# Kernel tuning notes

Hardware: AMD Instinct MI355X
Metric: run time of the kernel (lower is better)

The kernel has to match this reference:

```python
import jax, jax.numpy as jnp
import numpy as np

E = 768
H = 12
D = E // H  # head_dim = 64
EPS = 1e-6
SCALE = D ** -0.5


def _l2norm(x, eps=EPS):
    # torch F.normalize: x / clamp_min(||x||_2, eps)
    n = jnp.sqrt(jnp.sum(x * x, axis=-1, keepdims=True))
    return x / jnp.maximum(n, eps)


def setup_inputs() -> dict:
    key = jax.random.key(0)
    ks = jax.random.split(key, 12)
    B, S = 2, 2048
    w = lambda k: jax.random.normal(k, (E, E), dtype=jnp.float32) * 0.02
    b = lambda k: jax.random.normal(k, (E,), dtype=jnp.float32) * 0.02
    return {
        "query": jax.random.normal(ks[0], (B, S, E), dtype=jnp.float32),
        "key": jax.random.normal(ks[1], (B, S, E), dtype=jnp.float32),
        "value": jax.random.normal(ks[2], (B, S, E), dtype=jnp.float32),
        "Wq": w(ks[3]), "bq": b(ks[4]),
        "Wk": w(ks[5]), "bk": b(ks[6]),
        "Wv": w(ks[7]), "bv": b(ks[8]),
        "Wo": w(ks[9]), "bo": b(ks[10]),
    }


def reference(query, key, value, Wq, bq, Wk, bk, Wv, bv, Wo, bo):
    B, T, _ = query.shape
    S = key.shape[1]
    # nn.Linear: x @ W.T + b; then split heads -> [B, H, S, D]
    split = lambda x, L: x.reshape(B, L, H, D).transpose(0, 2, 1, 3)
    q = split(query @ Wq.T + bq, T)
    k = split(key @ Wk.T + bk, S)
    v = split(value @ Wv.T + bv, S)
    q = _l2norm(q)
    k = _l2norm(k)
    scores = jnp.einsum("bhtd,bhsd->bhts", q, k) * SCALE
    attn = jax.nn.softmax(scores, axis=-1)
    ctx = jnp.einsum("bhts,bhsd->bhtd", attn, v)
    ctx = ctx.transpose(0, 2, 1, 3).reshape(B, T, E)
    return ctx @ Wo.T + bo
```

## Files before the change

kernel.cpp:

```cpp
#include <hip/hip_runtime.h>
#include <hip/hip_bf16.h>

#define EE 768
#define HH 12
#define DD 64
#define BB 2
#define SS 2048
#define MM (BB*SS)

typedef short short8 __attribute__((ext_vector_type(8)));
typedef float f32x4 __attribute__((ext_vector_type(4)));

static __device__ __forceinline__ unsigned short f2bf(float f) {
    unsigned int u = __float_as_uint(f);
    u += 0x7fffu + ((u >> 16) & 1u);
    return (unsigned short)(u >> 16);
}

static __device__ __forceinline__ int swz(int row, int chunk) {
    return row * 128 + ((chunk ^ (row & 7)) << 4);
}

__global__ __launch_bounds__(256) void qkv_mfma_kernel(
    const float* __restrict__ xq, const float* __restrict__ xk, const float* __restrict__ xv,
    const float* __restrict__ Wq, const float* __restrict__ bq,
    const float* __restrict__ Wk, const float* __restrict__ bk,
    const float* __restrict__ Wv, const float* __restrict__ bv,
    unsigned short* __restrict__ qo, unsigned short* __restrict__ ko,
    unsigned short* __restrict__ vo)
{
    __shared__ short As[128 * 64];
    __shared__ short Bs[64 * 64];
    __shared__ float ssq[2][128];

    const int tid = threadIdx.x;
    const int bm  = blockIdx.x * 128;
    const int by  = blockIdx.y;
    const int proj = by / 12;
    const int h    = by % 12;
    const int n0r  = h * 64;

    const float* x    = (proj == 0) ? xq : (proj == 1) ? xk : xv;
    const float* W    = (proj == 0) ? Wq : (proj == 1) ? Wk : Wv;
    const float* bias = (proj == 0) ? bq : (proj == 1) ? bk : bv;

    const int w  = tid >> 6;
    const int l  = tid & 63;
    const int c  = l & 15;
    const int g  = l >> 4;
    const int wm = w >> 1;
    const int wn = w & 1;

    f32x4 acc[4][2] = {};

    for (int kt = 0; kt < EE; kt += 64) {
        __syncthreads();
        #pragma unroll
        for (int i = 0; i < 4; ++i) {
            const int cid = tid + 256 * i;
            const int row = cid >> 3, ch = cid & 7;
            const float* ga = x + (size_t)(bm + row) * EE + kt + ch * 8;
            float4 f0 = *(const float4*)ga;
            float4 f1 = *(const float4*)(ga + 4);
            short8 pk;
            pk[0]=f2bf(f0.x); pk[1]=f2bf(f0.y); pk[2]=f2bf(f0.z); pk[3]=f2bf(f0.w);
            pk[4]=f2bf(f1.x); pk[5]=f2bf(f1.y); pk[6]=f2bf(f1.z); pk[7]=f2bf(f1.w);
            *(short8*)((char*)As + swz(row, ch)) = pk;
        }
        #pragma unroll
        for (int i = 0; i < 2; ++i) {
            const int cid = tid + 256 * i;
            const int row = cid >> 3, ch = cid & 7;
            const float* ga = W + (size_t)(n0r + row) * EE + kt + ch * 8;
            float4 f0 = *(const float4*)ga;
            float4 f1 = *(const float4*)(ga + 4);
            short8 pk;
            pk[0]=f2bf(f0.x); pk[1]=f2bf(f0.y); pk[2]=f2bf(f0.z); pk[3]=f2bf(f0.w);
            pk[4]=f2bf(f1.x); pk[5]=f2bf(f1.y); pk[6]=f2bf(f1.z); pk[7]=f2bf(f1.w);
            *(short8*)((char*)Bs + swz(row, ch)) = pk;
        }
        __syncthreads();

        #pragma unroll
        for (int ks = 0; ks < 2; ++ks) {
            short8 bf[2], af[4];
            #pragma unroll
            for (int nt = 0; nt < 2; ++nt) {
                const int row = wn * 32 + nt * 16 + c;
                bf[nt] = *(const short8*)((const char*)Bs + swz(row, ks * 4 + g));
            }
            #pragma unroll
            for (int mt = 0; mt < 4; ++mt) {
                const int row = wm * 64 + mt * 16 + c;
                af[mt] = *(const short8*)((const char*)As + swz(row, ks * 4 + g));
            }
            #pragma unroll
            for (int mt = 0; mt < 4; ++mt)
                #pragma unroll
                for (int nt = 0; nt < 2; ++nt)
                    acc[mt][nt] = __builtin_amdgcn_mfma_f32_16x16x32_bf16(
                        af[mt], bf[nt], acc[mt][nt], 0, 0, 0);
        }
    }
    __syncthreads();

    float bb[2];
    #pragma unroll
    for (int nt = 0; nt < 2; ++nt) bb[nt] = bias[n0r + wn * 32 + nt * 16 + c];

    const int bidx = bm >> 11;
    const int sbase = bm & (SS - 1);

    if (proj < 2) {
        f32x4 vr[4][2];
        f32x4 ssp[4];
        #pragma unroll
        for (int mt = 0; mt < 4; ++mt) {
            #pragma unroll
            for (int nt = 0; nt < 2; ++nt)
                #pragma unroll
                for (int j = 0; j < 4; ++j)
                    vr[mt][nt][j] = acc[mt][nt][j] + bb[nt];
            #pragma unroll
            for (int j = 0; j < 4; ++j)
                ssp[mt][j] = vr[mt][0][j]*vr[mt][0][j] + vr[mt][1][j]*vr[mt][1][j];
            #pragma unroll
            for (int j = 0; j < 4; ++j) {
                float s = ssp[mt][j];
                #pragma unroll
                for (int msk = 1; msk < 16; msk <<= 1) s += __shfl_xor(s, msk);
                ssp[mt][j] = s;
            }
        }
        if (c == 0) {
            #pragma unroll
            for (int mt = 0; mt < 4; ++mt)
                #pragma unroll
                for (int j = 0; j < 4; ++j)
                    ssq[wn][wm * 64 + mt * 16 + g * 4 + j] = ssp[mt][j];
        }
        __syncthreads();
        unsigned short* dst = (proj == 0) ? qo : ko;
        const float fold = (proj == 0) ? 0.125f : 1.0f;
        #pragma unroll
        for (int mt = 0; mt < 4; ++mt) {
            #pragma unroll
            for (int j = 0; j < 4; ++j) {
                const int rloc = wm * 64 + mt * 16 + g * 4 + j;
                const float ss = ssq[0][rloc] + ssq[1][rloc];
                const float inv = fold / fmaxf(sqrtf(ss), 1e-6f);
                const size_t base =
                    ((size_t)(bidx * HH + h) * SS + sbase + rloc) * DD;
                #pragma unroll
                for (int nt = 0; nt < 2; ++nt)
                    dst[base + wn * 32 + nt * 16 + c] = f2bf(vr[mt][nt][j] * inv);
            }
        }
    } else {
        #pragma unroll
        for (int mt = 0; mt < 4; ++mt)
            #pragma unroll
            for (int nt = 0; nt < 2; ++nt)
                #pragma unroll
                for (int j = 0; j < 4; ++j) {
                    const int row = wm * 64 + mt * 16 + g * 4 + j;
                    const int col = wn * 32 + nt * 16 + c;
                    As[row * 64 + col] = (short)f2bf(acc[mt][nt][j] + bb[nt]);
                }
        __syncthreads();
        const int d  = tid & 63;
        const int sb = (tid >> 6) * 32;
        unsigned short* dstp = vo + ((size_t)(bidx * HH + h) * DD + d) * SS + sbase + sb;
        #pragma unroll
        for (int grp = 0; grp < 4; ++grp) {
            unsigned int wds[4];
            #pragma unroll
            for (int e = 0; e < 4; ++e) {
                unsigned short u0 = (unsigned short)As[(sb + grp * 8 + 2 * e)     * 64 + d];
                unsigned short u1 = (unsigned short)As[(sb + grp * 8 + 2 * e + 1) * 64 + d];
                wds[e] = (unsigned int)u0 | ((unsigned int)u1 << 16);
            }
            int4 pk = make_int4((int)wds[0], (int)wds[1], (int)wds[2], (int)wds[3]);
            *(int4*)(dstp + grp * 8) = pk;
        }
    }
}

__global__ __launch_bounds__(256) void attn_mfma_kernel(
    const unsigned short* __restrict__ q, const unsigned short* __restrict__ k,
    const unsigned short* __restrict__ vT, unsigned short* __restrict__ ctx)
{
    __shared__ short Ks[64 * 64];
    __shared__ short Vs[64 * 64];
    __shared__ short Ps[4 * 16 * 64];

    const int tid = threadIdx.x;
    const int bh  = blockIdx.y;
    const int w   = tid >> 6;
    const int l   = tid & 63;
    const int c   = l & 15;
    const int g   = l >> 4;
    const int qr0 = blockIdx.x * 64 + w * 16;

    const unsigned short* qg = q + ((size_t)bh * SS + qr0 + c) * DD;
    short8 aq[2];
    aq[0] = *(const short8*)(qg + g * 8);
    aq[1] = *(const short8*)(qg + 32 + g * 8);

    short* Psw = Ps + w * (16 * 64);

    f32x4 o[4] = {};
    f32x4 lr = {0.f, 0.f, 0.f, 0.f};

    for (int s0 = 0; s0 < SS; s0 += 64) {
        __syncthreads();
        #pragma unroll
        for (int i = 0; i < 2; ++i) {
            const int cid = tid + 256 * i;
            const int key = cid >> 3, ch = cid & 7;
            int4 kv4 = *(const int4*)(k + ((size_t)bh * SS + s0 + key) * DD + ch * 8);
            *(int4*)((char*)Ks + swz(key, ch)) = kv4;
        }
        #pragma unroll
        for (int i = 0; i < 2; ++i) {
            const int cid = tid + 256 * i;
            const int d = cid >> 3, ch = cid & 7;
            int4 vv4 = *(const int4*)(vT + ((size_t)bh * DD + d) * SS + s0 + ch * 8);
            *(int4*)((char*)Vs + swz(d, ch)) = vv4;
        }
        __syncthreads();

        f32x4 sc[4] = {};
        #pragma unroll
        for (int ks = 0; ks < 2; ++ks)
            #pragma unroll
            for (int nt = 0; nt < 4; ++nt) {
                const int row = nt * 16 + c;
                short8 kf = *(const short8*)((const char*)Ks + swz(row, ks * 4 + g));
                sc[nt] = __builtin_amdgcn_mfma_f32_16x16x32_bf16(aq[ks], kf, sc[nt], 0, 0, 0);
            }

        f32x4 p[4];
        #pragma unroll
        for (int nt = 0; nt < 4; ++nt)
            #pragma unroll
            for (int j = 0; j < 4; ++j)
                p[nt][j] = __expf(sc[nt][j]);
        f32x4 rs;
        #pragma unroll
        for (int j = 0; j < 4; ++j) {
            float r = p[0][j] + p[1][j] + p[2][j] + p[3][j];
            #pragma unroll
            for (int msk = 1; msk < 16; msk <<= 1) r += __shfl_xor(r, msk);
            rs[j] = r;
        }
        #pragma unroll
        for (int j = 0; j < 4; ++j) lr[j] += rs[j];

        #pragma unroll
        for (int nt = 0; nt < 4; ++nt)
            #pragma unroll
            for (int j = 0; j < 4; ++j) {
                const int row = g * 4 + j;
                const int elem = row * 64 + (((nt * 2 + (c >> 3)) ^ (row & 7)) << 3) + (c & 7);
                Psw[elem] = (short)f2bf(p[nt][j]);
            }

        #pragma unroll
        for (int ks = 0; ks < 2; ++ks) {
            short8 pa = *(const short8*)((const char*)Psw + swz(c, ks * 4 + g));
            #pragma unroll
            for (int dt = 0; dt < 4; ++dt) {
                const int row = dt * 16 + c;
                short8 vf = *(const short8*)((const char*)Vs + swz(row, ks * 4 + g));
                o[dt] = __builtin_amdgcn_mfma_f32_16x16x32_bf16(pa, vf, o[dt], 0, 0, 0);
            }
        }
    }

    const int bidx = bh / HH, h = bh % HH;
    f32x4 invl;
    #pragma unroll
    for (int j = 0; j < 4; ++j) invl[j] = 1.0f / lr[j];
    #pragma unroll
    for (int j = 0; j < 4; ++j) {
        const int sg = qr0 + g * 4 + j;
        unsigned short* op = ctx + ((size_t)bidx * SS + sg) * EE + h * DD + c;
        #pragma unroll
        for (int dt = 0; dt < 4; ++dt)
            op[dt * 16] = f2bf(o[dt][j] * invl[j]);
    }
}

__global__ __launch_bounds__(256) void out_mfma_kernel(
    const unsigned short* __restrict__ A, const float* __restrict__ W,
    const float* __restrict__ bias, float* __restrict__ out)
{
    __shared__ short As[128 * 64];
    __shared__ short Bs[64 * 64];

    const int tid = threadIdx.x;
    const int bm  = blockIdx.x * 128;
    const int n0  = blockIdx.y * 64;

    const int w  = tid >> 6;
    const int l  = tid & 63;
    const int c  = l & 15;
    const int g  = l >> 4;
    const int wm = w >> 1;
    const int wn = w & 1;

    f32x4 acc[4][2] = {};

    for (int kt = 0; kt < EE; kt += 64) {
        __syncthreads();
        #pragma unroll
        for (int i = 0; i < 4; ++i) {
            const int cid = tid + 256 * i;
            const int row = cid >> 3, ch = cid & 7;
            int4 a8 = *(const int4*)(A + (size_t)(bm + row) * EE + kt + ch * 8);
            *(int4*)((char*)As + swz(row, ch)) = a8;
        }
        #pragma unroll
        for (int i = 0; i < 2; ++i) {
            const int cid = tid + 256 * i;
            const int row = cid >> 3, ch = cid & 7;
            const float* ga = W + (size_t)(n0 + row) * EE + kt + ch * 8;
            float4 f0 = *(const float4*)ga;
            float4 f1 = *(const float4*)(ga + 4);
            short8 pk;
            pk[0]=f2bf(f0.x); pk[1]=f2bf(f0.y); pk[2]=f2bf(f0.z); pk[3]=f2bf(f0.w);
            pk[4]=f2bf(f1.x); pk[5]=f2bf(f1.y); pk[6]=f2bf(f1.z); pk[7]=f2bf(f1.w);
            *(short8*)((char*)Bs + swz(row, ch)) = pk;
        }
        __syncthreads();

        #pragma unroll
        for (int ks = 0; ks < 2; ++ks) {
            short8 bf[2], af[4];
            #pragma unroll
            for (int nt = 0; nt < 2; ++nt) {
                const int row = wn * 32 + nt * 16 + c;
                bf[nt] = *(const short8*)((const char*)Bs + swz(row, ks * 4 + g));
            }
            #pragma unroll
            for (int mt = 0; mt < 4; ++mt) {
                const int row = wm * 64 + mt * 16 + c;
                af[mt] = *(const short8*)((const char*)As + swz(row, ks * 4 + g));
            }
            #pragma unroll
            for (int mt = 0; mt < 4; ++mt)
                #pragma unroll
                for (int nt = 0; nt < 2; ++nt)
                    acc[mt][nt] = __builtin_amdgcn_mfma_f32_16x16x32_bf16(
                        af[mt], bf[nt], acc[mt][nt], 0, 0, 0);
        }
    }

    float bb[2];
    #pragma unroll
    for (int nt = 0; nt < 2; ++nt) bb[nt] = bias[n0 + wn * 32 + nt * 16 + c];

    #pragma unroll
    for (int mt = 0; mt < 4; ++mt)
        #pragma unroll
        for (int j = 0; j < 4; ++j) {
            const int row = bm + wm * 64 + mt * 16 + g * 4 + j;
            float* op = out + (size_t)row * EE + n0 + wn * 32 + c;
            #pragma unroll
            for (int nt = 0; nt < 2; ++nt)
                op[nt * 16] = acc[mt][nt][j] + bb[nt];
        }
}

extern "C" void kernel_launch(void* const* d_in, const int* in_sizes, int n_in,
                              void* d_out, int out_size, void* d_ws, size_t ws_size,
                              hipStream_t stream)
{
    const float* query = (const float*)d_in[0];
    const float* key   = (const float*)d_in[1];
    const float* value = (const float*)d_in[2];
    const float* Wq = (const float*)d_in[3];
    const float* bq = (const float*)d_in[4];
    const float* Wk = (const float*)d_in[5];
    const float* bk = (const float*)d_in[6];
    const float* Wv = (const float*)d_in[7];
    const float* bv = (const float*)d_in[8];
    const float* Wo = (const float*)d_in[9];
    const float* bo = (const float*)d_in[10];
    float* out = (float*)d_out;

    const size_t NQ = (size_t)BB * HH * SS * DD;
    unsigned short* qws  = (unsigned short*)d_ws;
    unsigned short* kws  = qws + NQ;
    unsigned short* vtws = kws + NQ;
    unsigned short* ctx  = vtws + NQ;

    qkv_mfma_kernel<<<dim3(MM/128, 36), 256, 0, stream>>>(
        query, key, value, Wq, bq, Wk, bk, Wv, bv, qws, kws, vtws);
    attn_mfma_kernel<<<dim3(SS/64, BB*HH), 256, 0, stream>>>(qws, kws, vtws, ctx);
    out_mfma_kernel<<<dim3(MM/128, EE/64), 256, 0, stream>>>(ctx, Wo, bo, out);
}
```

Measured before the change: 246.2 us.

## Pre-convert inputs to bf16, use direct global-to-LDS loads, widen attention waves

Adds separate kernels that convert activations and all four weight matrices to bf16 up front, so the GEMM kernels stop redoing fp32-to-bf16 conversion for every tile they reload. The GEMM and attention tile loads now use global_load_lds with an XOR-swizzled source column, replacing the register round-trip. The attention kernel drops to 128 threads, with each wave handling 32 query rows so each K/V fragment feeds two MFMAs. The cost is two extra launches, extra workspace traffic for the bf16 copies, and fewer waves per attention block.

```diff
diff --git a/kernel.cpp b/kernel.cpp
--- a/kernel.cpp
+++ b/kernel.cpp
@@ -7,6 +7,8 @@
 #define BB 2
 #define SS 2048
 #define MM (BB*SS)
+#define NT (MM*EE)
+#define NW (EE*EE)
 
 typedef short short8 __attribute__((ext_vector_type(8)));
 typedef float f32x4 __attribute__((ext_vector_type(4)));
@@ -17,15 +19,51 @@
     return (unsigned short)(u >> 16);
 }
 
+static __device__ __forceinline__ void gl16(const void* g, void* l) {
+    __builtin_amdgcn_global_load_lds(
+        (const __attribute__((address_space(1))) unsigned int*)g,
+        (__attribute__((address_space(3))) unsigned int*)l, 16, 0, 0);
+}
+
 static __device__ __forceinline__ int swz(int row, int chunk) {
     return row * 128 + ((chunk ^ (row & 7)) << 4);
 }
 
+__global__ __launch_bounds__(256) void cvt_x_kernel(
+    const float* __restrict__ a0, const float* __restrict__ a1, const float* __restrict__ a2,
+    unsigned short* __restrict__ o0, unsigned short* __restrict__ o1, unsigned short* __restrict__ o2)
+{
+    const float* s = (blockIdx.y == 0) ? a0 : (blockIdx.y == 1) ? a1 : a2;
+    unsigned short* d = (blockIdx.y == 0) ? o0 : (blockIdx.y == 1) ? o1 : o2;
+    const int idx = blockIdx.x * 256 + threadIdx.x;
+    float4 f = ((const float4*)s)[idx];
+    ushort4 u;
+    u.x = f2bf(f.x); u.y = f2bf(f.y); u.z = f2bf(f.z); u.w = f2bf(f.w);
+    ((ushort4*)d)[idx] = u;
+}
+
+__global__ __launch_bounds__(256) void cvt_w_kernel(
+    const float* __restrict__ a0, const float* __restrict__ a1,
+    const float* __restrict__ a2, const float* __restrict__ a3,
+    unsigned short* __restrict__ o0, unsigned short* __restrict__ o1,
+    unsigned short* __restrict__ o2, unsigned short* __restrict__ o3)
+{
+    const int y = blockIdx.y;
+    const float* s = (y == 0) ? a0 : (y == 1) ? a1 : (y == 2) ? a2 : a3;
+    unsigned short* d = (y == 0) ? o0 : (y == 1) ? o1 : (y == 2) ? o2 : o3;
+    const int idx = blockIdx.x * 256 + threadIdx.x;
+    float4 f = ((const float4*)s)[idx];
+    ushort4 u;
+    u.x = f2bf(f.x); u.y = f2bf(f.y); u.z = f2bf(f.z); u.w = f2bf(f.w);
+    ((ushort4*)d)[idx] = u;
+}
+
 __global__ __launch_bounds__(256) void qkv_mfma_kernel(
-    const float* __restrict__ xq, const float* __restrict__ xk, const float* __restrict__ xv,
-    const float* __restrict__ Wq, const float* __restrict__ bq,
-    const float* __restrict__ Wk, const float* __restrict__ bk,
-    const float* __restrict__ Wv, const float* __restrict__ bv,
+    const unsigned short* __restrict__ xq, const unsigned short* __restrict__ xk,
+    const unsigned short* __restrict__ xv,
+    const unsigned short* __restrict__ Wq, const float* __restrict__ bq,
+    const unsigned short* __restrict__ Wk, const float* __restrict__ bk,
+    const unsigned short* __restrict__ Wv, const float* __restrict__ bv,
     unsigned short* __restrict__ qo, unsigned short* __restrict__ ko,
     unsigned short* __restrict__ vo)
 {
@@ -40,9 +78,9 @@
     const int h    = by % 12;
     const int n0r  = h * 64;
 
-    const float* x    = (proj == 0) ? xq : (proj == 1) ? xk : xv;
-    const float* W    = (proj == 0) ? Wq : (proj == 1) ? Wk : Wv;
-    const float* bias = (proj == 0) ? bq : (proj == 1) ? bk : bv;
+    const unsigned short* x = (proj == 0) ? xq : (proj == 1) ? xk : xv;
+    const unsigned short* W = (proj == 0) ? Wq : (proj == 1) ? Wk : Wv;
+    const float* bias       = (proj == 0) ? bq : (proj == 1) ? bk : bv;
 
     const int w  = tid >> 6;
     const int l  = tid & 63;
@@ -50,6 +88,8 @@
     const int g  = l >> 4;
     const int wm = w >> 1;
     const int wn = w & 1;
+    const int lr8 = l >> 3;
+    const int lc8 = (l & 7) ^ lr8;
 
     f32x4 acc[4][2] = {};
 
@@ -57,49 +97,35 @@
         __syncthreads();
         #pragma unroll
         for (int i = 0; i < 4; ++i) {
-            const int cid = tid + 256 * i;
-            const int row = cid >> 3, ch = cid & 7;
-            const float* ga = x + (size_t)(bm + row) * EE + kt + ch * 8;
-            float4 f0 = *(const float4*)ga;
-            float4 f1 = *(const float4*)(ga + 4);
-            short8 pk;
-            pk[0]=f2bf(f0.x); pk[1]=f2bf(f0.y); pk[2]=f2bf(f0.z); pk[3]=f2bf(f0.w);
-            pk[4]=f2bf(f1.x); pk[5]=f2bf(f1.y); pk[6]=f2bf(f1.z); pk[7]=f2bf(f1.w);
-            *(short8*)((char*)As + swz(row, ch)) = pk;
+            const int t = w * 4 + i;
+            const int row = t * 8 + lr8;
+            gl16(x + (size_t)(bm + row) * EE + kt + lc8 * 8,
+                 (unsigned short*)As + t * 512);
         }
         #pragma unroll
         for (int i = 0; i < 2; ++i) {
-            const int cid = tid + 256 * i;
-            const int row = cid >> 3, ch = cid & 7;
-            const float* ga = W + (size_t)(n0r + row) * EE + kt + ch * 8;
-            float4 f0 = *(const float4*)ga;
-            float4 f1 = *(const float4*)(ga + 4);
-            short8 pk;
-            pk[0]=f2bf(f0.x); pk[1]=f2bf(f0.y); pk[2]=f2bf(f0.z); pk[3]=f2bf(f0.w);
-            pk[4]=f2bf(f1.x); pk[5]=f2bf(f1.y); pk[6]=f2bf(f1.z); pk[7]=f2bf(f1.w);
-            *(short8*)((char*)Bs + swz(row, ch)) = pk;
+            const int t = w * 2 + i;
+            const int row = t * 8 + lr8;
+            gl16(W + (size_t)(n0r + row) * EE + kt + lc8 * 8,
+                 (unsigned short*)Bs + t * 512);
         }
         __syncthreads();
 
         #pragma unroll
         for (int ks = 0; ks < 2; ++ks) {
-            short8 bf[2], af[4];
-            #pragma unroll
-            for (int nt = 0; nt < 2; ++nt) {
-                const int row = wn * 32 + nt * 16 + c;
-                bf[nt] = *(const short8*)((const char*)Bs + swz(row, ks * 4 + g));
-            }
-            #pragma unroll
-            for (int mt = 0; mt < 4; ++mt) {
-                const int row = wm * 64 + mt * 16 + c;
-                af[mt] = *(const short8*)((const char*)As + swz(row, ks * 4 + g));
-            }
+            short8 bfr[2], afr[4];
+            #pragma unroll
+            for (int nt = 0; nt < 2; ++nt)
+                bfr[nt] = *(const short8*)((const char*)Bs + swz(wn * 32 + nt * 16 + c, ks * 4 + g));
+            #pragma unroll
+            for (int mt = 0; mt < 4; ++mt)
+                afr[mt] = *(const short8*)((const char*)As + swz(wm * 64 + mt * 16 + c, ks * 4 + g));
             #pragma unroll
             for (int mt = 0; mt < 4; ++mt)
                 #pragma unroll
                 for (int nt = 0; nt < 2; ++nt)
                     acc[mt][nt] = __builtin_amdgcn_mfma_f32_16x16x32_bf16(
-                        af[mt], bf[nt], acc[mt][nt], 0, 0, 0);
+                        afr[mt], bfr[nt], acc[mt][nt], 0, 0, 0);
         }
     }
     __syncthreads();
@@ -108,7 +134,7 @@
     #pragma unroll
     for (int nt = 0; nt < 2; ++nt) bb[nt] = bias[n0r + wn * 32 + nt * 16 + c];
 
-    const int bidx = bm >> 11;
+    const int bidx  = bm >> 11;
     const int sbase = bm & (SS - 1);
 
     if (proj < 2) {
@@ -186,13 +212,13 @@
     }
 }
 
-__global__ __launch_bounds__(256) void attn_mfma_kernel(
+__global__ __launch_bounds__(128) void attn_mfma_kernel(
     const unsigned short* __restrict__ q, const unsigned short* __restrict__ k,
     const unsigned short* __restrict__ vT, unsigned short* __restrict__ ctx)
 {
     __shared__ short Ks[64 * 64];
     __shared__ short Vs[64 * 64];
-    __shared__ short Ps[4 * 16 * 64];
+    __shared__ short Ps[2 * 32 * 64];
 
     const int tid = threadIdx.x;
     const int bh  = blockIdx.y;
@@ -200,100 +226,108 @@
     const int l   = tid & 63;
     const int c   = l & 15;
     const int g   = l >> 4;
-    const int qr0 = blockIdx.x * 64 + w * 16;
-
-    const unsigned short* qg = q + ((size_t)bh * SS + qr0 + c) * DD;
-    short8 aq[2];
-    aq[0] = *(const short8*)(qg + g * 8);
-    aq[1] = *(const short8*)(qg + 32 + g * 8);
-
-    short* Psw = Ps + w * (16 * 64);
-
-    f32x4 o[4] = {};
-    f32x4 lr = {0.f, 0.f, 0.f, 0.f};
+    const int lr8 = l >> 3;
+    const int lc8 = (l & 7) ^ lr8;
+    const int qr0 = blockIdx.x * 64 + w * 32;
+
+    short8 aq[2][2];
+    #pragma unroll
+    for (int m = 0; m < 2; ++m) {
+        const unsigned short* qg = q + ((size_t)bh * SS + qr0 + m * 16 + c) * DD;
+        aq[m][0] = *(const short8*)(qg + g * 8);
+        aq[m][1] = *(const short8*)(qg + 32 + g * 8);
+    }
+
+    short* Psw = Ps + w * (32 * 64);
+    f32x4 o[2][4] = {};
+    f32x4 lsum[2] = {};
 
     for (int s0 = 0; s0 < SS; s0 += 64) {
         __syncthreads();
         #pragma unroll
-        for (int i = 0; i < 2; ++i) {
-            const int cid = tid + 256 * i;
-            const int key = cid >> 3, ch = cid & 7;
-            int4 kv4 = *(const int4*)(k + ((size_t)bh * SS + s0 + key) * DD + ch * 8);
-            *(int4*)((char*)Ks + swz(key, ch)) = kv4;
-        }
-        #pragma unroll
-        for (int i = 0; i < 2; ++i) {
-            const int cid = tid + 256 * i;
-            const int d = cid >> 3, ch = cid & 7;
-            int4 vv4 = *(const int4*)(vT + ((size_t)bh * DD + d) * SS + s0 + ch * 8);
-            *(int4*)((char*)Vs + swz(d, ch)) = vv4;
-        }
-        __syncthreads();
-
-        f32x4 sc[4] = {};
+        for (int i = 0; i < 4; ++i) {
+            const int t = w * 4 + i;
+            gl16(k + ((size_t)bh * SS + s0 + t * 8 + lr8) * DD + lc8 * 8,
+                 (unsigned short*)Ks + t * 512);
+        }
+        #pragma unroll
+        for (int i = 0; i < 4; ++i) {
+            const int t = w * 4 + i;
+            gl16(vT + ((size_t)bh * DD + t * 8 + lr8) * SS + s0 + lc8 * 8,
+                 (unsigned short*)Vs + t * 512);
+        }
+        __syncthreads();
+
+        f32x4 sc[2][4] = {};
         #pragma unroll
         for (int ks = 0; ks < 2; ++ks)
             #pragma unroll
             for (int nt = 0; nt < 4; ++nt) {
-                const int row = nt * 16 + c;
-                short8 kf = *(const short8*)((const char*)Ks + swz(row, ks * 4 + g));
-                sc[nt] = __builtin_amdgcn_mfma_f32_16x16x32_bf16(aq[ks], kf, sc[nt], 0, 0, 0);
-            }
-
-        f32x4 p[4];
-        #pragma unroll
-        for (int nt = 0; nt < 4; ++nt)
-            #pragma unroll
-            for (int j = 0; j < 4; ++j)
-                p[nt][j] = __expf(sc[nt][j]);
-        f32x4 rs;
+                short8 kf = *(const short8*)((const char*)Ks + swz(nt * 16 + c, ks * 4 + g));
+                #pragma unroll
+                for (int m = 0; m < 2; ++m)
+                    sc[m][nt] = __builtin_amdgcn_mfma_f32_16x16x32_bf16(
+                        aq[m][ks], kf, sc[m][nt], 0, 0, 0);
+            }
+
+        #pragma unroll
+        for (int m = 0; m < 2; ++m) {
+            f32x4 p[4];
+            #pragma unroll
+            for (int nt = 0; nt < 4; ++nt)
+                #pragma unroll
+                for (int j = 0; j < 4; ++j)
+                    p[nt][j] = __expf(sc[m][nt][j]);
+            #pragma unroll
+            for (int j = 0; j < 4; ++j) {
+                float r = p[0][j] + p[1][j] + p[2][j] + p[3][j];
+                #pragma unroll
+                for (int msk = 1; msk < 16; msk <<= 1) r += __shfl_xor(r, msk);
+                lsum[m][j] += r;
+            }
+            #pragma unroll
+            for (int nt = 0; nt < 4; ++nt)
+                #pragma unroll
+                for (int j = 0; j < 4; ++j) {
+                    const int row = m * 16 + g * 4 + j;
+                    const int ch  = (nt * 2 + (c >> 3)) ^ (row & 7);
+                    Psw[row * 64 + (ch << 3) + (c & 7)] = (short)f2bf(p[nt][j]);
+                }
+        }
+
+        #pragma unroll
+        for (int ks = 0; ks < 2; ++ks) {
+            short8 pa[2];
+            #pragma unroll
+            for (int m = 0; m < 2; ++m)
+                pa[m] = *(const short8*)((const char*)Psw + swz(m * 16 + c, ks * 4 + g));
+            #pragma unroll
+            for (int dt = 0; dt < 4; ++dt) {
+                short8 vf = *(const short8*)((const char*)Vs + swz(dt * 16 + c, ks * 4 + g));
+                #pragma unroll
+                for (int m = 0; m < 2; ++m)
+                    o[m][dt] = __builtin_amdgcn_mfma_f32_16x16x32_bf16(
+                        pa[m], vf, o[m][dt], 0, 0, 0);
+            }
+        }
+    }
+
+    const int bidx = bh / HH, h = bh % HH;
+    #pragma unroll
+    for (int m = 0; m < 2; ++m)
         #pragma unroll
         for (int j = 0; j < 4; ++j) {
-            float r = p[0][j] + p[1][j] + p[2][j] + p[3][j];
-            #pragma unroll
-            for (int msk = 1; msk < 16; msk <<= 1) r += __shfl_xor(r, msk);
-            rs[j] = r;
-        }
-        #pragma unroll
-        for (int j = 0; j < 4; ++j) lr[j] += rs[j];
-
-        #pragma unroll
-        for (int nt = 0; nt < 4; ++nt)
-            #pragma unroll
-            for (int j = 0; j < 4; ++j) {
-                const int row = g * 4 + j;
-                const int elem = row * 64 + (((nt * 2 + (c >> 3)) ^ (row & 7)) << 3) + (c & 7);
-                Psw[elem] = (short)f2bf(p[nt][j]);
-            }
-
-        #pragma unroll
-        for (int ks = 0; ks < 2; ++ks) {
-            short8 pa = *(const short8*)((const char*)Psw + swz(c, ks * 4 + g));
-            #pragma unroll
-            for (int dt = 0; dt < 4; ++dt) {
-                const int row = dt * 16 + c;
-                short8 vf = *(const short8*)((const char*)Vs + swz(row, ks * 4 + g));
-                o[dt] = __builtin_amdgcn_mfma_f32_16x16x32_bf16(pa, vf, o[dt], 0, 0, 0);
-            }
-        }
-    }
-
-    const int bidx = bh / HH, h = bh % HH;
-    f32x4 invl;
-    #pragma unroll
-    for (int j = 0; j < 4; ++j) invl[j] = 1.0f / lr[j];
-    #pragma unroll
-    for (int j = 0; j < 4; ++j) {
-        const int sg = qr0 + g * 4 + j;
-        unsigned short* op = ctx + ((size_t)bidx * SS + sg) * EE + h * DD + c;
-        #pragma unroll
-        for (int dt = 0; dt < 4; ++dt)
-            op[dt * 16] = f2bf(o[dt][j] * invl[j]);
-    }
+            const float inv = 1.0f / lsum[m][j];
+            const int sg = qr0 + m * 16 + g * 4 + j;
+            unsigned short* op = ctx + ((size_t)bidx * SS + sg) * EE + h * DD + c;
+            #pragma unroll
+            for (int dt = 0; dt < 4; ++dt)
+                op[dt * 16] = f2bf(o[m][dt][j] * inv);
+        }
 }
 
 __global__ __launch_bounds__(256) void out_mfma_kernel(
-    const unsigned short* __restrict__ A, const float* __restrict__ W,
+    const unsigned short* __restrict__ A, const unsigned short* __restrict__ W,
     const float* __restrict__ bias, float* __restrict__ out)
 {
     __shared__ short As[128 * 64];
@@ -309,6 +343,8 @@
     const int g  = l >> 4;
     const int wm = w >> 1;
     const int wn = w & 1;
+    const int lr8 = l >> 3;
+    const int lc8 = (l & 7) ^ lr8;
 
     f32x4 acc[4][2] = {};
 
@@ -316,44 +352,35 @@
         __syncthreads();
         #pragma unroll
         for (int i = 0; i < 4; ++i) {
-            const int cid = tid + 256 * i;
-            const int row = cid >> 3, ch = cid & 7;
-            int4 a8 = *(const int4*)(A + (size_t)(bm + row) * EE + kt + ch * 8);
-            *(int4*)((char*)As + swz(row, ch)) = a8;
+            const int t = w * 4 + i;
+            const int row = t * 8 + lr8;
+            gl16(A + (size_t)(bm + row) * EE + kt + lc8 * 8,
+                 (unsigned short*)As + t * 512);
         }
         #pragma unroll
         for (int i = 0; i < 2; ++i) {
-            const int cid = tid + 256 * i;
-            const int row = cid >> 3, ch = cid & 7;
-            const float* ga = W + (size_t)(n0 + row) * EE + kt + ch * 8;
-            float4 f0 = *(const float4*)ga;
-            float4 f1 = *(const float4*)(ga + 4);
-            short8 pk;
-            pk[0]=f2bf(f0.x); pk[1]=f2bf(f0.y); pk[2]=f2bf(f0.z); pk[3]=f2bf(f0.w);
-            pk[4]=f2bf(f1.x); pk[5]=f2bf(f1.y); pk[6]=f2bf(f1.z); pk[7]=f2bf(f1.w);
-            *(short8*)((char*)Bs + swz(row, ch)) = pk;
+            const int t = w * 2 + i;
+            const int row = t * 8 + lr8;
+            gl16(W + (size_t)(n0 + row) * EE + kt + lc8 * 8,
+                 (unsigned short*)Bs + t * 512);
         }
         __syncthreads();
 
         #pragma unroll
         for (int ks = 0; ks < 2; ++ks) {
-            short8 bf[2], af[4];
-            #pragma unroll
-            for (int nt = 0; nt < 2; ++nt) {
-                const int row = wn * 32 + nt * 16 + c;
-                bf[nt] = *(const short8*)((const char*)Bs + swz(row, ks * 4 + g));
-            }
-            #pragma unroll
-            for (int mt = 0; mt < 4; ++mt) {
-                const int row = wm * 64 + mt * 16 + c;
-                af[mt] = *(const short8*)((const char*)As + swz(row, ks * 4 + g));
-            }
+            short8 bfr[2], afr[4];
+            #pragma unroll
+            for (int nt = 0; nt < 2; ++nt)
+                bfr[nt] = *(const short8*)((const char*)Bs + swz(wn * 32 + nt * 16 + c, ks * 4 + g));
+            #pragma unroll
+            for (int mt = 0; mt < 4; ++mt)
+                afr[mt] = *(const short8*)((const char*)As + swz(wm * 64 + mt * 16 + c, ks * 4 + g));
             #pragma unroll
             for (int mt = 0; mt < 4; ++mt)
                 #pragma unroll
                 for (int nt = 0; nt < 2; ++nt)
                     acc[mt][nt] = __builtin_amdgcn_mfma_f32_16x16x32_bf16(
-                        af[mt], bf[nt], acc[mt][nt], 0, 0, 0);
+                        afr[mt], bfr[nt], acc[mt][nt], 0, 0, 0);
         }
     }
 
@@ -390,14 +417,26 @@
     const float* bo = (const float*)d_in[10];
     float* out = (float*)d_out;
 
-    const size_t NQ = (size_t)BB * HH * SS * DD;
-    unsigned short* qws  = (unsigned short*)d_ws;
-    unsigned short* kws  = qws + NQ;
-    unsigned short* vtws = kws + NQ;
-    unsigned short* ctx  = vtws + NQ;
-
-    qkv_mfma_kernel<<<dim3(MM/128, 36), 256, 0, stream>>>(
-        query, key, value, Wq, bq, Wk, bk, Wv, bv, qws, kws, vtws);
-    attn_mfma_kernel<<<dim3(SS/64, BB*HH), 256, 0, stream>>>(qws, kws, vtws, ctx);
-    out_mfma_kernel<<<dim3(MM/128, EE/64), 256, 0, stream>>>(ctx, Wo, bo, out);
-}
+    unsigned short* xqc  = (unsigned short*)d_ws;
+    unsigned short* xkc  = xqc  + NT;
+    unsigned short* xvc  = xkc  + NT;
+    unsigned short* qws  = xvc  + NT;
+    unsigned short* kws  = qws  + NT;
+    unsigned short* vtws = kws  + NT;
+    unsigned short* wqc  = vtws + NT;
+    unsigned short* wkc  = wqc  + NW;
+    unsigned short* wvc  = wkc  + NW;
+    unsigned short* woc  = wvc  + NW;
+    unsigned short* ctx  = xqc;
+
+    cvt_x_kernel<<<dim3(NT / 4 / 256, 3), 256, 0, stream>>>(
+        query, key, value, xqc, xkc, xvc);
+    cvt_w_kernel<<<dim3(NW / 4 / 256, 4), 256, 0, stream>>>(
+        Wq, Wk, Wv, Wo, wqc, wkc, wvc, woc);
+    qkv_mfma_kernel<<<dim3(MM / 128, 36), 256, 0, stream>>>(
+        xqc, xkc, xvc, wqc, bq, wkc, bk, wvc, bv, qws, kws, vtws);
+    attn_mfma_kernel<<<dim3(SS / 64, BB * HH), 128, 0, stream>>>(
+        qws, kws, vtws, ctx);
+    out_mfma_kernel<<<dim3(MM / 128, EE / 64), 256, 0, stream>>>(
+        ctx, woc, bo, out);
+}
```

Measured after the change: 235.2 us. -4.5%, faster.
